# Optimization experiments

Hardware: AMD Instinct MI355X
Metric: run time of the kernel (lower is better)

## Reference

```python
import jax, jax.numpy as jnp
import numpy as np

EPS = 1e-08


def setup_inputs() -> dict:
    key = jax.random.key(0)
    student_output = jax.random.normal(key, (8192, 1024), dtype=jnp.float32)
    return {"student_output": student_output}


def reference(student_output) -> jnp.ndarray:
    # F.normalize(p=2, dim=-1, eps=EPS): x / max(||x||_2, eps)
    x = student_output.astype(jnp.float32)
    norm = jnp.linalg.norm(x, axis=-1, keepdims=True)
    x = x / jnp.maximum(norm, EPS)

    n = x.shape[0]
    # full similarity matrix with diagonal masked to -1.0 (self-sim excluded)
    sim = x @ x.T  # [N, N]
    sim = jnp.where(jnp.eye(n, dtype=bool), jnp.float32(-1.0), sim)
    indices = jnp.argmax(sim, axis=1)  # nearest neighbor per row

    # torch.nn.PairwiseDistance(2, eps): ||x1 - x2 + eps||_2 along feature dim
    diff = x - x[indices] + EPS
    distances = jnp.sqrt(jnp.sum(diff * diff, axis=-1))

    return -jnp.mean(jnp.log(distances + EPS))
```

## Files before the change

### kernel.cpp

```cpp
#include <hip/hip_runtime.h>
#include <stdint.h>

#define N 8192
#define DIM 1024
#define EPSF 1e-8f
#define NBLK 32
#define NTRI 528
#define NKT 32

typedef __attribute__((ext_vector_type(4))) float f32x4;
typedef __attribute__((ext_vector_type(8))) short s16x8;

__device__ inline unsigned short f2bf(float f) {
  unsigned u = __float_as_uint(f);
  unsigned r = (u + 0x7FFFu + ((u >> 16) & 1u)) >> 16;
  return (unsigned short)r;
}

__device__ inline unsigned encf(float f) {
  unsigned u = __float_as_uint(f);
  return (u & 0x80000000u) ? ~u : (u | 0x80000000u);
}

#define XB_OFF   0
#define INV_OFF  16777216
#define KEY_OFF  16809984
#define PART_OFF 16875520

__global__ __launch_bounds__(256)
void k_norm(const float* __restrict__ x, unsigned short* __restrict__ xb,
            float* __restrict__ invn, unsigned long long* __restrict__ keys) {
  int row = blockIdx.x, t = threadIdx.x;
  const float4* xr = (const float4*)(x + (size_t)row * DIM);
  float4 v = xr[t];
  float ss = v.x * v.x + v.y * v.y + v.z * v.z + v.w * v.w;
#pragma unroll
  for (int o = 32; o > 0; o >>= 1) ss += __shfl_down(ss, o, 64);
  __shared__ float red[4];
  __shared__ float sinv;
  if ((t & 63) == 0) red[t >> 6] = ss;
  __syncthreads();
  if (t == 0) {
    float s = red[0] + red[1] + red[2] + red[3];
    float inv = 1.0f / fmaxf(sqrtf(s), EPSF);
    sinv = inv;
    invn[row] = inv;
    keys[row] = 0ull;
  }
  __syncthreads();
  float inv = sinv;
  ushort4 o4;
  o4.x = f2bf(v.x * inv);
  o4.y = f2bf(v.y * inv);
  o4.z = f2bf(v.z * inv);
  o4.w = f2bf(v.w * inv);
  ((ushort4*)(xb + (size_t)row * DIM))[t] = o4;
}

__global__ __launch_bounds__(512, 2)
void k_sim(const unsigned short* __restrict__ xb, unsigned long long* __restrict__ keys) {
  extern __shared__ unsigned short lds_us[];

  int b = blockIdx.x;
  int bi = (int)((65.0f - sqrtf(4225.0f - 8.0f * (float)b)) * 0.5f);
  while ((bi + 1) * (65 - (bi + 1)) / 2 <= b) ++bi;
  while (bi * (65 - bi) / 2 > b) --bi;
  int bj = bi + (b - bi * (65 - bi) / 2);

  const int t = threadIdx.x, lane = t & 63, wv = t >> 6;
  const int wr = wv >> 2, wc = wv & 3;
  const int hi = lane >> 4, lo = lane & 15;
  const int rowBase = bi * 256, colBase = bj * 256;

  const unsigned short* gA = xb + (size_t)rowBase * DIM;
  const unsigned short* gB = xb + (size_t)colBase * DIM;

  const int sg = (lane & 3) ^ ((lane >> 3) & 3);
  const size_t soA0 = (size_t)(wv * 16 + (lane >> 2)) * DIM + sg * 8;
  const size_t soA1 = soA0 + (size_t)128 * DIM;
  const int ldsA0 = wv * 512;
  const int ldsA1 = 4096 + wv * 512;

#define STAGE_TILE(tt) do {                                                          \
    const size_t ko_ = (size_t)(tt) * 32;                                            \
    unsigned short* Ab_ = lds_us + ((tt) & 3) * 8192;                                \
    unsigned short* Bb_ = lds_us + 32768 + ((tt) & 3) * 8192;                        \
    __builtin_amdgcn_global_load_lds(                                                \
        (const __attribute__((address_space(1))) void*)(gA + soA0 + ko_),            \
        (__attribute__((address_space(3))) void*)(Ab_ + ldsA0), 16, 0, 0);           \
    __builtin_amdgcn_global_load_lds(                                                \
        (const __attribute__((address_space(1))) void*)(gA + soA1 + ko_),            \
        (__attribute__((address_space(3))) void*)(Ab_ + ldsA1), 16, 0, 0);           \
    __builtin_amdgcn_global_load_lds(                                                \
        (const __attribute__((address_space(1))) void*)(gB + soA0 + ko_),            \
        (__attribute__((address_space(3))) void*)(Bb_ + ldsA0), 16, 0, 0);           \
    __builtin_amdgcn_global_load_lds(                                                \
        (const __attribute__((address_space(1))) void*)(gB + soA1 + ko_),            \
        (__attribute__((address_space(3))) void*)(Bb_ + ldsA1), 16, 0, 0);           \
  } while (0)

  const f32x4 fzero = {0.f, 0.f, 0.f, 0.f};
  f32x4 acc[8][4];
#pragma unroll
  for (int i = 0; i < 8; ++i)
#pragma unroll
    for (int j = 0; j < 4; ++j) acc[i][j] = fzero;

  const int chux = (hi ^ ((lo >> 1) & 3)) * 8;

  STAGE_TILE(0);
  STAGE_TILE(1);
  STAGE_TILE(2);
  asm volatile("s_waitcnt vmcnt(8)" ::: "memory");
  asm volatile("s_barrier" ::: "memory");

  for (int kt = 0; kt < NKT; ++kt) {
    if (kt < NKT - 3) STAGE_TILE(kt + 3);

    const unsigned short* Ab = lds_us + (kt & 3) * 8192;
    const unsigned short* Bb = lds_us + 32768 + (kt & 3) * 8192;
    s16x8 af[8], bfr[4];
#pragma unroll
    for (int mi = 0; mi < 8; ++mi) {
      int r = wr * 128 + mi * 16 + lo;
      af[mi] = *(const s16x8*)(Ab + r * 32 + chux);
    }
#pragma unroll
    for (int ni = 0; ni < 4; ++ni) {
      int r = wc * 64 + ni * 16 + lo;
      bfr[ni] = *(const s16x8*)(Bb + r * 32 + chux);
    }

    __builtin_amdgcn_s_setprio(1);
#pragma unroll
    for (int mi = 0; mi < 8; ++mi)
#pragma unroll
      for (int ni = 0; ni < 4; ++ni)
        acc[mi][ni] = __builtin_amdgcn_mfma_f32_16x16x32_bf16(af[mi], bfr[ni], acc[mi][ni], 0, 0, 0);
    __builtin_amdgcn_s_setprio(0);

    if (kt < NKT - 3) asm volatile("s_waitcnt vmcnt(8)" ::: "memory");
    else              asm volatile("s_waitcnt vmcnt(0)" ::: "memory");
    asm volatile("s_barrier" ::: "memory");
  }
#undef STAGE_TILE

#pragma unroll
  for (int am = 0; am < 8; ++am) {
#pragma unroll
    for (int reg = 0; reg < 4; ++reg) {
      int grow = rowBase + wr * 128 + am * 16 + hi * 4 + reg;
      float best = -10.0f;
      int bcol = 0;
#pragma unroll
      for (int ni = 0; ni < 4; ++ni) {
        int gcol = colBase + wc * 64 + ni * 16 + lo;
        float v = acc[am][ni][reg];
        v = (gcol == grow) ? -10.0f : v;
        if (v > best || (v == best && gcol < bcol)) { best = v; bcol = gcol; }
      }
#pragma unroll
      for (int m = 1; m < 16; m <<= 1) {
        float ov = __shfl_xor(best, m, 64);
        int oc = __shfl_xor(bcol, m, 64);
        if (ov > best || (ov == best && oc < bcol)) { best = ov; bcol = oc; }
      }
      if (lo == 0) {
        unsigned long long key = ((unsigned long long)encf(best) << 32) | (unsigned)(~bcol);
        atomicMax(&keys[grow], key);
      }
    }
  }

  if (bi != bj) {
#pragma unroll
    for (int ni = 0; ni < 4; ++ni) {
      int gcol = colBase + wc * 64 + ni * 16 + lo;
      float best = -10.0f;
      int brow = 0;
#pragma unroll
      for (int am = 0; am < 8; ++am)
#pragma unroll
        for (int reg = 0; reg < 4; ++reg) {
          int grow = rowBase + wr * 128 + am * 16 + hi * 4 + reg;
          float v = acc[am][ni][reg];
          if (v > best || (v == best && grow < brow)) { best = v; brow = grow; }
        }
#pragma unroll
      for (int m = 16; m < 64; m <<= 1) {
        float ov = __shfl_xor(best, m, 64);
        int oc = __shfl_xor(brow, m, 64);
        if (ov > best || (ov == best && oc < brow)) { best = ov; brow = oc; }
      }
      if (hi == 0) {
        unsigned long long key = ((unsigned long long)encf(best) << 32) | (unsigned)(~brow);
        atomicMax(&keys[gcol], key);
      }
    }
  }
}

__global__ __launch_bounds__(256)
void k_dist(const float* __restrict__ x, const float* __restrict__ invn,
            const unsigned long long* __restrict__ keys, float* __restrict__ part) {
  int row = blockIdx.x, t = threadIdx.x;
  unsigned long long key = keys[row];
  int nb = (int)(~(unsigned)key);
  float ia = invn[row], ib = invn[nb];
  float4 a = ((const float4*)(x + (size_t)row * DIM))[t];
  float4 b = ((const float4*)(x + (size_t)nb * DIM))[t];
  float d0 = a.x * ia - b.x * ib + EPSF;
  float d1 = a.y * ia - b.y * ib + EPSF;
  float d2 = a.z * ia - b.z * ib + EPSF;
  float d3 = a.w * ia - b.w * ib + EPSF;
  float ss = d0 * d0 + d1 * d1 + d2 * d2 + d3 * d3;
#pragma unroll
  for (int o = 32; o > 0; o >>= 1) ss += __shfl_down(ss, o, 64);
  __shared__ float red[4];
  if ((t & 63) == 0) red[t >> 6] = ss;
  __syncthreads();
  if (t == 0) {
    float s = red[0] + red[1] + red[2] + red[3];
    part[row] = logf(sqrtf(s) + EPSF);
  }
}

__global__ __launch_bounds__(1024)
void k_final(const float* __restrict__ part, float* __restrict__ out) {
  int t = threadIdx.x;
  float s = 0.0f;
#pragma unroll
  for (int i = 0; i < N / 1024; ++i) s += part[t + i * 1024];
#pragma unroll
  for (int o = 32; o > 0; o >>= 1) s += __shfl_down(s, o, 64);
  __shared__ float red[16];
  if ((t & 63) == 0) red[t >> 6] = s;
  __syncthreads();
  if (t == 0) {
    float tot = 0.0f;
#pragma unroll
    for (int i = 0; i < 16; ++i) tot += red[i];
    out[0] = -tot / (float)N;
  }
}

extern "C" void kernel_launch(void* const* d_in, const int* in_sizes, int n_in,
                              void* d_out, int out_size, void* d_ws, size_t ws_size,
                              hipStream_t stream) {
  const float* x = (const float*)d_in[0];
  float* out = (float*)d_out;
  char* ws = (char*)d_ws;
  unsigned short* xb = (unsigned short*)(ws + XB_OFF);
  float* invn = (float*)(ws + INV_OFF);
  unsigned long long* keys = (unsigned long long*)(ws + KEY_OFF);
  float* part = (float*)(ws + PART_OFF);

  (void)hipFuncSetAttribute((const void*)k_sim,
                            hipFuncAttributeMaxDynamicSharedMemorySize, 131072);

  k_norm<<<N, 256, 0, stream>>>(x, xb, invn, keys);
  k_sim<<<NTRI, 512, 131072, stream>>>(xb, keys);
  k_dist<<<N, 256, 0, stream>>>(x, invn, keys, part);
  k_final<<<1, 1024, 0, stream>>>(part, out);
}
```

Measured before the change: 239.9 us.

## Restructure sim GEMM into double-buffered K=64 tiles with interleaved quarter-staged loads

The similarity GEMM main loop changes from a 4-stage ring of K=32 tiles to a 2-buffer scheme with K=64 tiles (16 iterations). Each tile is computed in four MFMA quadrants, and the next tile's global-to-LDS loads are split into halves issued between them, with barriers and setprio around each phase. The LDS swizzle is redone for 64-element rows. The __launch_bounds__ occupancy hint of 2 is dropped. This aims to overlap loads with MFMA work in a ping-pong style, at the cost of more barriers, a shallower prefetch depth and a full vmcnt(0) wait at the end of every tile.

```diff
diff --git a/kernel.cpp b/kernel.cpp
--- a/kernel.cpp
+++ b/kernel.cpp
@@ -6,7 +6,7 @@
 #define EPSF 1e-8f
 #define NBLK 32
 #define NTRI 528
-#define NKT 32
+#define KT 16
 
 typedef __attribute__((ext_vector_type(4))) float f32x4;
 typedef __attribute__((ext_vector_type(8))) short s16x8;
@@ -57,7 +57,7 @@
   ((ushort4*)(xb + (size_t)row * DIM))[t] = o4;
 }
 
-__global__ __launch_bounds__(512, 2)
+__global__ __launch_bounds__(512)
 void k_sim(const unsigned short* __restrict__ xb, unsigned long long* __restrict__ keys) {
   extern __shared__ unsigned short lds_us[];
 
@@ -75,28 +75,22 @@
   const unsigned short* gA = xb + (size_t)rowBase * DIM;
   const unsigned short* gB = xb + (size_t)colBase * DIM;
 
-  const int sg = (lane & 3) ^ ((lane >> 3) & 3);
-  const size_t soA0 = (size_t)(wv * 16 + (lane >> 2)) * DIM + sg * 8;
-  const size_t soA1 = soA0 + (size_t)128 * DIM;
-  const int ldsA0 = wv * 512;
-  const int ldsA1 = 4096 + wv * 512;
-
-#define STAGE_TILE(tt) do {                                                          \
-    const size_t ko_ = (size_t)(tt) * 32;                                            \
-    unsigned short* Ab_ = lds_us + ((tt) & 3) * 8192;                                \
-    unsigned short* Bb_ = lds_us + 32768 + ((tt) & 3) * 8192;                        \
+  const int srow = t >> 3;
+  const int schunk = (t & 7) ^ (srow & 7);
+  const size_t so0 = (size_t)srow * DIM + schunk * 8;
+  const size_t so1 = (size_t)(64 + srow) * DIM + schunk * 8;
+  const int ld0 = t * 8;
+  const int ld1 = 4096 + t * 8;
+
+#define STAGE_HALF(GP, OPLDS, NB, H, T_) do {                                        \
+    const size_t gbase = (size_t)(H) * 128 * DIM + (size_t)(T_) * 64;                \
+    unsigned short* lb = lds_us + (OPLDS) + (NB) * 16384 + (H) * 8192;               \
     __builtin_amdgcn_global_load_lds(                                                \
-        (const __attribute__((address_space(1))) void*)(gA + soA0 + ko_),            \
-        (__attribute__((address_space(3))) void*)(Ab_ + ldsA0), 16, 0, 0);           \
+        (const __attribute__((address_space(1))) void*)(GP + gbase + so0),           \
+        (__attribute__((address_space(3))) void*)(lb + ld0), 16, 0, 0);              \
     __builtin_amdgcn_global_load_lds(                                                \
-        (const __attribute__((address_space(1))) void*)(gA + soA1 + ko_),            \
-        (__attribute__((address_space(3))) void*)(Ab_ + ldsA1), 16, 0, 0);           \
-    __builtin_amdgcn_global_load_lds(                                                \
-        (const __attribute__((address_space(1))) void*)(gB + soA0 + ko_),            \
-        (__attribute__((address_space(3))) void*)(Bb_ + ldsA0), 16, 0, 0);           \
-    __builtin_amdgcn_global_load_lds(                                                \
-        (const __attribute__((address_space(1))) void*)(gB + soA1 + ko_),            \
-        (__attribute__((address_space(3))) void*)(Bb_ + ldsA1), 16, 0, 0);           \
+        (const __attribute__((address_space(1))) void*)(GP + gbase + so1),           \
+        (__attribute__((address_space(3))) void*)(lb + ld1), 16, 0, 0);              \
   } while (0)
 
   const f32x4 fzero = {0.f, 0.f, 0.f, 0.f};
@@ -106,44 +100,84 @@
 #pragma unroll
     for (int j = 0; j < 4; ++j) acc[i][j] = fzero;
 
-  const int chux = (hi ^ ((lo >> 1) & 3)) * 8;
-
-  STAGE_TILE(0);
-  STAGE_TILE(1);
-  STAGE_TILE(2);
-  asm volatile("s_waitcnt vmcnt(8)" ::: "memory");
-  asm volatile("s_barrier" ::: "memory");
-
-  for (int kt = 0; kt < NKT; ++kt) {
-    if (kt < NKT - 3) STAGE_TILE(kt + 3);
-
-    const unsigned short* Ab = lds_us + (kt & 3) * 8192;
-    const unsigned short* Bb = lds_us + 32768 + (kt & 3) * 8192;
-    s16x8 af[8], bfr[4];
-#pragma unroll
-    for (int mi = 0; mi < 8; ++mi) {
-      int r = wr * 128 + mi * 16 + lo;
-      af[mi] = *(const s16x8*)(Ab + r * 32 + chux);
-    }
-#pragma unroll
-    for (int ni = 0; ni < 4; ++ni) {
-      int r = wc * 64 + ni * 16 + lo;
-      bfr[ni] = *(const s16x8*)(Bb + r * 32 + chux);
-    }
-
-    __builtin_amdgcn_s_setprio(1);
-#pragma unroll
-    for (int mi = 0; mi < 8; ++mi)
-#pragma unroll
-      for (int ni = 0; ni < 4; ++ni)
-        acc[mi][ni] = __builtin_amdgcn_mfma_f32_16x16x32_bf16(af[mi], bfr[ni], acc[mi][ni], 0, 0, 0);
-    __builtin_amdgcn_s_setprio(0);
-
-    if (kt < NKT - 3) asm volatile("s_waitcnt vmcnt(8)" ::: "memory");
-    else              asm volatile("s_waitcnt vmcnt(0)" ::: "memory");
-    asm volatile("s_barrier" ::: "memory");
-  }
-#undef STAGE_TILE
+  const int l7 = lo & 7;
+
+#define RD(BASE_, R_, KK_) (*(const s16x8*)(lds_us + (BASE_) + (R_) * 64 + ((((KK_) << 2) | hi) ^ l7) * 8))
+
+#define BAR __builtin_amdgcn_s_barrier()
+
+#define TILE(CB, T_, DS) do {                                                        \
+    const int Ab = (CB) * 16384, Bb = 32768 + (CB) * 16384, NB = (CB) ^ 1;           \
+    s16x8 af[4][2], b01[2][2], b23[2][2];                                            \
+                                             \
+    _Pragma("unroll") for (int mi = 0; mi < 4; ++mi)                                 \
+      _Pragma("unroll") for (int kk = 0; kk < 2; ++kk)                               \
+        af[mi][kk] = RD(Ab, wr * 128 + mi * 16 + lo, kk);                            \
+    _Pragma("unroll") for (int ni = 0; ni < 2; ++ni)                                 \
+      _Pragma("unroll") for (int kk = 0; kk < 2; ++kk)                               \
+        b01[ni][kk] = RD(Bb, wc * 64 + ni * 16 + lo, kk);                            \
+    if (DS) { STAGE_HALF(gA, 0, NB, 0, (T_) + 1); STAGE_HALF(gA, 0, NB, 1, (T_) + 1); } \
+    BAR;                                                                             \
+    __builtin_amdgcn_s_setprio(1);                                                   \
+    _Pragma("unroll") for (int mi = 0; mi < 4; ++mi)                                 \
+      _Pragma("unroll") for (int ni = 0; ni < 2; ++ni)                               \
+        _Pragma("unroll") for (int kk = 0; kk < 2; ++kk)                             \
+          acc[mi][ni] = __builtin_amdgcn_mfma_f32_16x16x32_bf16(af[mi][kk], b01[ni][kk], acc[mi][ni], 0, 0, 0); \
+    __builtin_amdgcn_s_setprio(0);                                                   \
+    BAR;                                                                             \
+                                             \
+    _Pragma("unroll") for (int ni = 0; ni < 2; ++ni)                                 \
+      _Pragma("unroll") for (int kk = 0; kk < 2; ++kk)                               \
+        b23[ni][kk] = RD(Bb, wc * 64 + (ni + 2) * 16 + lo, kk);                      \
+    if (DS) STAGE_HALF(gB, 32768, NB, 0, (T_) + 1);                                  \
+    BAR;                                                                             \
+    __builtin_amdgcn_s_setprio(1);                                                   \
+    _Pragma("unroll") for (int mi = 0; mi < 4; ++mi)                                 \
+      _Pragma("unroll") for (int ni = 0; ni < 2; ++ni)                               \
+        _Pragma("unroll") for (int kk = 0; kk < 2; ++kk)                             \
+          acc[mi][ni + 2] = __builtin_amdgcn_mfma_f32_16x16x32_bf16(af[mi][kk], b23[ni][kk], acc[mi][ni + 2], 0, 0, 0); \
+    __builtin_amdgcn_s_setprio(0);                                                   \
+    BAR;                                                                             \
+                                             \
+    _Pragma("unroll") for (int mi = 0; mi < 4; ++mi)                                 \
+      _Pragma("unroll") for (int kk = 0; kk < 2; ++kk)                               \
+        af[mi][kk] = RD(Ab, wr * 128 + (mi + 4) * 16 + lo, kk);                      \
+    if (DS) STAGE_HALF(gB, 32768, NB, 1, (T_) + 1);                                  \
+    BAR;                                                                             \
+    __builtin_amdgcn_s_setprio(1);                                                   \
+    _Pragma("unroll") for (int mi = 0; mi < 4; ++mi)                                 \
+      _Pragma("unroll") for (int ni = 0; ni < 2; ++ni)                               \
+        _Pragma("unroll") for (int kk = 0; kk < 2; ++kk)                             \
+          acc[mi + 4][ni + 2] = __builtin_amdgcn_mfma_f32_16x16x32_bf16(af[mi][kk], b23[ni][kk], acc[mi + 4][ni + 2], 0, 0, 0); \
+    __builtin_amdgcn_s_setprio(0);                                                   \
+    BAR;                                                                             \
+                               \
+    __builtin_amdgcn_s_setprio(1);                                                   \
+    _Pragma("unroll") for (int mi = 0; mi < 4; ++mi)                                 \
+      _Pragma("unroll") for (int ni = 0; ni < 2; ++ni)                               \
+        _Pragma("unroll") for (int kk = 0; kk < 2; ++kk)                             \
+          acc[mi + 4][ni] = __builtin_amdgcn_mfma_f32_16x16x32_bf16(af[mi][kk], b01[ni][kk], acc[mi + 4][ni], 0, 0, 0); \
+    __builtin_amdgcn_s_setprio(0);                                                   \
+    asm volatile("s_waitcnt vmcnt(0)" ::: "memory");   \
+    BAR;                                                                             \
+  } while (0)
+
+  STAGE_HALF(gA, 0, 0, 0, 0); STAGE_HALF(gA, 0, 0, 1, 0);
+  STAGE_HALF(gB, 32768, 0, 0, 0); STAGE_HALF(gB, 32768, 0, 1, 0);
+  asm volatile("s_waitcnt vmcnt(0)" ::: "memory");
+  BAR;
+
+  for (int kb = 0; kb < 14; kb += 2) {
+    TILE(0, kb, 1);
+    TILE(1, kb + 1, 1);
+  }
+  TILE(0, 14, 1);
+  TILE(1, 15, 0);
+
+#undef TILE
+#undef RD
+#undef BAR
+#undef STAGE_HALF
 
 #pragma unroll
   for (int am = 0; am < 8; ++am) {
```

Result: faster. 234.6 us (-2.2%).
